# Kernel optimization log

Measured on AMD Instinct MI355X. Metric: run time of the kernel, lower is better.

## Reference

```python
import jax, jax.numpy as jnp
import numpy as np

B, W, D, R = 8, 1024, 1024, 64
GAMMA_MIN, GAMMA_MAX, ALPHA_CAP, EPS = 0.15, 1.0, 1.0, 1e-8


def _linear_init(key, fan_in, shape):
    bound = 1.0 / np.sqrt(fan_in)
    return jax.random.uniform(key, shape, jnp.float32, -bound, bound)


def setup_inputs() -> dict:
    key = jax.random.key(0)
    ks = jax.random.split(key, 12)
    h = jax.random.normal(ks[0], (B, W, D), jnp.float32)
    # k_base init as in __init__: exp(-0.15*max(j-i,0)) * tril, row-normalized
    pos = jnp.arange(W, dtype=jnp.float32)
    dist_ji = jnp.clip(pos[None, :] - pos[:, None], 0.0)
    causal = jnp.tril(jnp.ones((W, W), jnp.float32))
    k_init = jnp.exp(-0.15 * dist_ji) * causal
    k_base = k_init / jnp.clip(k_init.sum(axis=1, keepdims=True), 1e-8)
    # decay_logit init: gammas in [0.95, 0.995] -> inverse sigmoid of normalized gamma
    gammas = jnp.linspace(0.95, 0.995, R)
    graw = jnp.clip((gammas - GAMMA_MIN) / (GAMMA_MAX - GAMMA_MIN), 1e-6, 1 - 1e-6)
    decay_logit = jnp.log(graw / (1.0 - graw))
    return {
        "h": h,
        "k_base": k_base,
        "decay_logit": decay_logit,
        "gate_logit": jnp.asarray(8.0, jnp.float32),
        "alpha_logit": jnp.asarray(0.0, jnp.float32),
        "u": 0.05 * jax.random.normal(ks[1], (D, R), jnp.float32),
        "v": 0.05 * jax.random.normal(ks[2], (D, R), jnp.float32),
        "proj_w": _linear_init(ks[3], D, (D, D)),
        "proj_b": _linear_init(ks[4], D, (D,)),
        "norm1_scale": jnp.ones((D,), jnp.float32),
        "norm2_scale": jnp.ones((D,), jnp.float32),
        "up_w": _linear_init(ks[5], D, (2 * D, D)),
        "up_b": _linear_init(ks[6], D, (2 * D,)),
        "down_w": _linear_init(ks[7], 2 * D, (D, 2 * D)),
        "down_b": _linear_init(ks[8], 2 * D, (D,)),
    }


def _rmsnorm(x, scale):
    return x * jax.lax.rsqrt(jnp.mean(x * x, axis=-1, keepdims=True) + 1e-8) * scale


def _l2norm(x):
    # mirrors F.normalize(x, dim=-1, eps=1e-8)
    n = jnp.sqrt(jnp.sum(x * x, axis=-1, keepdims=True))
    return x / jnp.maximum(n, EPS)


def reference(h, k_base, decay_logit, gate_logit, alpha_logit, u, v,
              proj_w, proj_b, norm1_scale, norm2_scale,
              up_w, up_b, down_w, down_b):
    _, w, _ = h.shape
    pos = jnp.arange(w, dtype=h.dtype)
    causal = jnp.tril(jnp.ones((w, w), h.dtype))          # [W, W]
    dist = jnp.clip(pos[:, None] - pos[None, :], 0.0)     # i - j, clamped >= 0

    residual = h
    h_norm = _rmsnorm(h, norm1_scale)

    # dense k_base path (k_base_rank == 0)
    gate = jax.nn.sigmoid(gate_logit)
    kb = k_base[:w, :w] * causal
    out = gate * jnp.einsum('ij,bjd->bid', kb, h_norm)

    # low-rank q/k with per-rank gamma decay (decay_impl='mask')
    qk = h_norm @ jnp.concatenate((u, v), axis=1)          # [B, W, 2R]
    q_raw, k_raw = jnp.split(qk, [u.shape[1]], axis=-1)
    q = _l2norm(q_raw)
    k = _l2norm(k_raw)

    gamma = GAMMA_MIN + (GAMMA_MAX - GAMMA_MIN) * jax.nn.sigmoid(decay_logit)  # [R]
    log_gamma = jnp.log(jnp.clip(gamma, 1e-8))
    decay_mask = jnp.exp(dist[:, :, None] * log_gamma[None, None, :]) * causal[:, :, None]  # [W, W, R]

    alpha = ALPHA_CAP * jax.nn.sigmoid(alpha_logit)
    # scores[b,i,j] = sum_r q[b,i,r] * decay[i,j,r] * k[b,j,r]
    scores = jnp.einsum('bir,ijr,bjr->bij', q, decay_mask, k)
    out = out + alpha * jnp.einsum('bij,bjd->bid', scores, h_norm)

    h1 = residual + (out @ proj_w.T + proj_b)
    # MLP (GELU exact, mult=2), second residual
    m = _rmsnorm(h1, norm2_scale)
    m = jax.nn.gelu(m @ up_w.T + up_b, approximate=False) @ down_w.T + down_b
    return h1 + m
```

## Files before the change

### kernel.cpp

```cpp
#include <hip/hip_runtime.h>
#include <hip/hip_bf16.h>
#include <math.h>

#define B_ 8
#define W_ 1024
#define D_ 1024
#define R_ 64

typedef __hip_bfloat16 bf16;
typedef __attribute__((ext_vector_type(8))) short bf16x8;
typedef __attribute__((ext_vector_type(4))) float f32x4;

__device__ __forceinline__ float tof(bf16 x) { return __bfloat162float(x); }
__device__ __forceinline__ short f2bs(float f) {
    bf16 b = __float2bfloat16(f);
    return *(short*)&b;
}

__device__ __forceinline__ void async16(const void* g, void* l) {
    __builtin_amdgcn_global_load_lds(
        (const __attribute__((address_space(1))) unsigned int*)g,
        (__attribute__((address_space(3))) unsigned int*)l,
        16, 0, 0);
}

__global__ __launch_bounds__(256)
void rmsnorm_kernel(const float* __restrict__ src, const float* __restrict__ scale,
                    bf16* __restrict__ dst) {
    int row = blockIdx.x;
    const float* x = src + (size_t)row * D_;
    bf16* y = dst + (size_t)row * D_;
    float xv[4];
    float ss = 0.f;
#pragma unroll
    for (int it = 0; it < 4; ++it) {
        int d = threadIdx.x + it * 256;
        xv[it] = x[d];
        ss += xv[it] * xv[it];
    }
#pragma unroll
    for (int off = 32; off; off >>= 1) ss += __shfl_down(ss, off, 64);
    __shared__ float red[4];
    __shared__ float invs;
    int lane = threadIdx.x & 63, wid = threadIdx.x >> 6;
    if (lane == 0) red[wid] = ss;
    __syncthreads();
    if (threadIdx.x == 0) {
        float t = red[0] + red[1] + red[2] + red[3];
        invs = rsqrtf(t / (float)D_ + 1e-8f);
    }
    __syncthreads();
    float inv = invs;
#pragma unroll
    for (int it = 0; it < 4; ++it) {
        int d = threadIdx.x + it * 256;
        y[d] = __float2bfloat16(xv[it] * inv * scale[d]);
    }
}

__global__ __launch_bounds__(256)
void transpose_kernel(const bf16* __restrict__ src, bf16* __restrict__ dst) {
    int b = blockIdx.z;
    int j0 = blockIdx.x * 64, d0 = blockIdx.y * 64;
    __shared__ short Ts[64][72];
    const bf16* S = src + (size_t)b * W_ * D_;
    bf16* Dd = dst + (size_t)b * W_ * D_;
    int tid = threadIdx.x;
    int r = tid >> 3, c = (tid & 7) * 8;
#pragma unroll
    for (int p = 0; p < 2; ++p) {
        int j = r + p * 32;
        bf16x8 vv = *(const bf16x8*)&S[(size_t)(j0 + j) * D_ + d0 + c];
#pragma unroll
        for (int e = 0; e < 8; ++e) Ts[j][c + e] = vv[e];
    }
    __syncthreads();
#pragma unroll
    for (int p = 0; p < 2; ++p) {
        int d = r + p * 32;
        bf16x8 vv;
#pragma unroll
        for (int e = 0; e < 8; ++e) vv[e] = Ts[c + e][d];
        *(bf16x8*)&Dd[(size_t)(d0 + d) * W_ + j0 + c] = vv;
    }
}

__global__ __launch_bounds__(256)
void uvT_kernel(const float* __restrict__ u, const float* __restrict__ v,
                bf16* __restrict__ uvT) {
    int g = blockIdx.z;
    int d0 = blockIdx.x * 64;
    const float* src = g ? v : u;
    __shared__ float Ts[64][65];
    int tid = threadIdx.x;
#pragma unroll
    for (int e = 0; e < 16; ++e) {
        int idx = tid + e * 256;
        int drow = idx >> 6, rcol = idx & 63;
        Ts[drow][rcol] = src[(size_t)(d0 + drow) * 64 + rcol];
    }
    __syncthreads();
#pragma unroll
    for (int e = 0; e < 16; ++e) {
        int idx = tid + e * 256;
        int orow = idx >> 6, ocol = idx & 63;
        uvT[(size_t)(g * 64 + orow) * D_ + d0 + ocol] = __float2bfloat16(Ts[ocol][orow]);
    }
}

__global__ __launch_bounds__(256)
void convert3_kernel(const float* __restrict__ proj, const float* __restrict__ up,
                     const float* __restrict__ down,
                     bf16* __restrict__ projb, bf16* __restrict__ upb,
                     bf16* __restrict__ downb) {
    size_t idx = ((size_t)blockIdx.x * 256 + threadIdx.x) * 8;
    const size_t DD = (size_t)D_ * D_;
    const float* src; bf16* dst; size_t off;
    if (idx < DD)          { src = proj; dst = projb; off = idx; }
    else if (idx < 3 * DD) { src = up;   dst = upb;   off = idx - DD; }
    else                   { src = down; dst = downb; off = idx - 3 * DD; }
    float4 f0 = *(const float4*)(src + off);
    float4 f1 = *(const float4*)(src + off + 4);
    bf16x8 p;
    p[0] = f2bs(f0.x); p[1] = f2bs(f0.y); p[2] = f2bs(f0.z); p[3] = f2bs(f0.w);
    p[4] = f2bs(f1.x); p[5] = f2bs(f1.y); p[6] = f2bs(f1.z); p[7] = f2bs(f1.w);
    *(bf16x8*)(dst + off) = p;
}

__global__ __launch_bounds__(128)
void qk_epilogue_kernel(const float* __restrict__ qkraw,
                        const float* __restrict__ decay_logit,
                        float* __restrict__ qg, float* __restrict__ kg) {
    int row = blockIdx.x;
    int i = row & (W_ - 1);
    int t = threadIdx.x;
    int r = t & 63;
    bool isK = t >= 64;
    const size_t PS = (size_t)B_ * W_ * 128;
    size_t off = (size_t)row * 128 + t;
    float val = qkraw[off] + qkraw[PS + off] + qkraw[2 * PS + off] + qkraw[3 * PS + off];
    float sq = val * val;
#pragma unroll
    for (int o = 32; o; o >>= 1) sq += __shfl_xor(sq, o, 64);
    val = val / fmaxf(sqrtf(sq), 1e-8f);

    float dl = decay_logit[r];
    float gamma = 0.15f + 0.85f * (1.f / (1.f + expf(-dl)));
    float lg = logf(gamma);
    float e = isK ? expf(-(float)i * lg) : expf((float)i * lg);
    float o = val * e;
    if (isK) kg[(size_t)row * R_ + r] = o;
    else     qg[(size_t)row * R_ + r] = o;
}

__global__ __launch_bounds__(256)
void buildM_kernel(const float* __restrict__ qg, const float* __restrict__ kg,
                   const float* __restrict__ k_base,
                   const float* __restrict__ gate_logit,
                   const float* __restrict__ alpha_logit,
                   bf16* __restrict__ M) {
    int b = blockIdx.z;
    int ti = blockIdx.y, tj = blockIdx.x;
    int i0 = ti * 32, j0 = tj * 32;
    int tx = threadIdx.x, ty = threadIdx.y;
    bf16* Mb = M + (size_t)b * W_ * W_;
    const bf16 zero = __float2bfloat16(0.f);

    if (tj > ti) {
#pragma unroll
        for (int a = 0; a < 2; ++a)
#pragma unroll
            for (int c = 0; c < 2; ++c)
                Mb[(size_t)(i0 + ty * 2 + a) * W_ + (j0 + tx * 2 + c)] = zero;
        return;
    }

    __shared__ float Qs[32][65];
    __shared__ float Ks[32][65];
    int tid = ty * 16 + tx;
    for (int e = tid; e < 32 * 64; e += 256) {
        int rr = e & 63, row = e >> 6;
        Qs[row][rr] = qg[((size_t)b * W_ + i0 + row) * R_ + rr];
        Ks[row][rr] = kg[((size_t)b * W_ + j0 + row) * R_ + rr];
    }
    __syncthreads();

    float acc[2][2] = {{0.f, 0.f}, {0.f, 0.f}};
#pragma unroll 8
    for (int r = 0; r < 64; ++r) {
        float qa = Qs[ty * 2 + 0][r], qb = Qs[ty * 2 + 1][r];
        float ka = Ks[tx * 2 + 0][r], kb = Ks[tx * 2 + 1][r];
        acc[0][0] += qa * ka; acc[0][1] += qa * kb;
        acc[1][0] += qb * ka; acc[1][1] += qb * kb;
    }

    float gate  = 1.f / (1.f + expf(-(*gate_logit)));
    float alpha = 1.f / (1.f + expf(-(*alpha_logit)));
#pragma unroll
    for (int a = 0; a < 2; ++a) {
#pragma unroll
        for (int c = 0; c < 2; ++c) {
            int i = i0 + ty * 2 + a, j = j0 + tx * 2 + c;
            float vkb = k_base[(size_t)i * W_ + j];
            float out = (j <= i) ? (gate * vkb + alpha * acc[a][c]) : 0.f;
            Mb[(size_t)i * W_ + j] = __float2bfloat16(out);
        }
    }
}

template<int EPI, int SK>
__global__ __launch_bounds__(512)
void mgemm_kernel(const bf16* __restrict__ A, const bf16* __restrict__ Bm,
                  const float* __restrict__ Res, const float* __restrict__ bias,
                  void* __restrict__ Cout,
                  int M, int N, int K,
                  long sA, long sB, long sC, int causal) {
    __shared__ __align__(16) short At[2][128 * 32];
    __shared__ __align__(16) short Bt[2][128 * 32];
    int z = blockIdx.z;
    const bf16* Ab = (SK > 1) ? A : A + (size_t)z * sA;
    const bf16* Bb = (SK > 1) ? Bm : Bm + (size_t)z * sB;
    int kchunk = K / SK;
    int kbeg = (SK > 1) ? z * kchunk : 0;
    int m0 = blockIdx.x * 128, n0 = blockIdx.y * 128;
    int tid = threadIdx.x;
    int lane = tid & 63, wave = tid >> 6;
    int wy = wave >> 1, wx = wave & 1;
    int quad = lane >> 4, l15 = lane & 15;

    f32x4 acc[2][4];
#pragma unroll
    for (int i = 0; i < 2; ++i)
#pragma unroll
        for (int j = 0; j < 4; ++j)
            acc[i][j] = (f32x4){0.f, 0.f, 0.f, 0.f};

    int kend = kbeg + kchunk;
    if (SK == 1 && causal) kend = (m0 + 128 < K) ? m0 + 128 : K;
    int nIter = (kend - kbeg) >> 5;

    int srcChunk = ((lane & 3) ^ ((lane >> 3) & 3)) * 8;
    size_t rowA = (size_t)(m0 + wave * 16 + (lane >> 2)) * K;
    size_t rowB = (size_t)(n0 + wave * 16 + (lane >> 2)) * K;
    const bf16* aP = Ab + rowA + srcChunk + kbeg;
    const bf16* bP = Bb + rowB + srcChunk + kbeg;
    short* dA[2] = { &At[0][wave * 512], &At[1][wave * 512] };
    short* dB[2] = { &Bt[0][wave * 512], &Bt[1][wave * 512] };

    int rswz = (quad ^ ((l15 >> 1) & 3)) * 8;

    async16(aP, dA[0]);
    async16(bP, dB[0]);
    aP += 32; bP += 32;
    __syncthreads();

    for (int it = 0; it < nIter; ++it) {
        int cur = it & 1;
        if (it + 1 < nIter) {
            int nxt = cur ^ 1;
            async16(aP, dA[nxt]);
            async16(bP, dB[nxt]);
            aP += 32; bP += 32;
        }
        bf16x8 af[2], bfr[4];
#pragma unroll
        for (int mi = 0; mi < 2; ++mi)
            af[mi] = *(const bf16x8*)&At[cur][(wy * 32 + mi * 16 + l15) * 32 + rswz];
#pragma unroll
        for (int ni = 0; ni < 4; ++ni)
            bfr[ni] = *(const bf16x8*)&Bt[cur][(wx * 64 + ni * 16 + l15) * 32 + rswz];
#pragma unroll
        for (int mi = 0; mi < 2; ++mi)
#pragma unroll
            for (int ni = 0; ni < 4; ++ni)
                acc[mi][ni] = __builtin_amdgcn_mfma_f32_16x16x32_bf16(
                    af[mi], bfr[ni], acc[mi][ni], 0, 0, 0);
        __syncthreads();
    }

#pragma unroll
    for (int ni = 0; ni < 4; ++ni) {
        int col = n0 + wx * 64 + ni * 16 + l15;
        float bv = (EPI == 1 || EPI == 2) ? bias[col] : 0.f;
#pragma unroll
        for (int mi = 0; mi < 2; ++mi) {
            int row0 = m0 + wy * 32 + mi * 16 + quad * 4;
#pragma unroll
            for (int r = 0; r < 4; ++r) {
                size_t idx = (size_t)(row0 + r) * N + col;
                float val = acc[mi][ni][r];
                if constexpr (EPI == 0) {
                    ((bf16*)Cout)[(size_t)z * sC + idx] = __float2bfloat16(val);
                } else if constexpr (EPI == 1) {
                    ((float*)Cout)[idx] = val + bv + Res[idx];
                } else if constexpr (EPI == 2) {
                    val += bv;
                    val = 0.5f * val * (1.f + erff(val * 0.70710678118654752f));
                    ((bf16*)Cout)[idx] = __float2bfloat16(val);
                } else {
                    ((float*)Cout)[(size_t)z * sC + idx] = val;
                }
            }
        }
    }
}

extern "C" void kernel_launch(void* const* d_in, const int* in_sizes, int n_in,
                              void* d_out, int out_size, void* d_ws, size_t ws_size,
                              hipStream_t stream) {
    const float* h           = (const float*)d_in[0];
    const float* k_base      = (const float*)d_in[1];
    const float* decay_logit = (const float*)d_in[2];
    const float* gate_logit  = (const float*)d_in[3];
    const float* alpha_logit = (const float*)d_in[4];
    const float* u           = (const float*)d_in[5];
    const float* v           = (const float*)d_in[6];
    const float* proj_w      = (const float*)d_in[7];
    const float* proj_b      = (const float*)d_in[8];
    const float* norm1_scale = (const float*)d_in[9];
    const float* norm2_scale = (const float*)d_in[10];
    const float* up_w        = (const float*)d_in[11];
    const float* up_b        = (const float*)d_in[12];
    const float* down_w      = (const float*)d_in[13];
    const float* down_b      = (const float*)d_in[14];

    const size_t MB = 1048576;
    char* ws = (char*)d_ws;
    bf16*  hnorm   = (bf16*)(ws);
    bf16*  uvT     = (bf16*)(ws + 16 * MB);
    float* qg      = (float*)(ws + 16 * MB);
    float* kg      = (float*)(ws + 18 * MB);
    bf16*  hnormT  = (bf16*)(ws + 20 * MB);
    float* qkraw   = (float*)(ws + 36 * MB);
    bf16*  Mbuf    = (bf16*)(ws + 36 * MB);
    bf16*  proj_wb = (bf16*)(ws + 52 * MB);
    bf16*  up_wb   = (bf16*)(ws + 54 * MB);
    bf16*  down_wb = (bf16*)(ws + 58 * MB);
    bf16*  attn    = hnorm;
    bf16*  mnorm   = hnorm;
    bf16*  tbuf    = hnormT;
    float* h1      = (float*)d_out;

    convert3_kernel<<<5 * D_ * D_ / 2048, 256, 0, stream>>>(
        proj_w, up_w, down_w, proj_wb, up_wb, down_wb);
    uvT_kernel<<<dim3(D_ / 64, 1, 2), 256, 0, stream>>>(u, v, uvT);

    rmsnorm_kernel<<<B_ * W_, 256, 0, stream>>>(h, norm1_scale, hnorm);

    transpose_kernel<<<dim3(W_ / 64, D_ / 64, B_), 256, 0, stream>>>(hnorm, hnormT);

    mgemm_kernel<5, 4><<<dim3(B_ * W_ / 128, 1, 4), 512, 0, stream>>>(
        hnorm, uvT, nullptr, nullptr, qkraw, B_ * W_, 128, D_,
        0, 0, (long)B_ * W_ * 128, 0);

    qk_epilogue_kernel<<<B_ * W_, 128, 0, stream>>>(qkraw, decay_logit, qg, kg);

    buildM_kernel<<<dim3(W_ / 32, W_ / 32, B_), dim3(16, 16), 0, stream>>>(
        qg, kg, k_base, gate_logit, alpha_logit, Mbuf);

    mgemm_kernel<0, 1><<<dim3(W_ / 128, D_ / 128, B_), 512, 0, stream>>>(
        Mbuf, hnormT, nullptr, nullptr, attn, W_, D_, W_,
        (long)W_ * W_, (long)W_ * D_, (long)W_ * D_, 1);

    mgemm_kernel<1, 1><<<dim3(B_ * W_ / 128, D_ / 128, 1), 512, 0, stream>>>(
        attn, proj_wb, h, proj_b, h1, B_ * W_, D_, D_, 0, 0, 0, 0);

    rmsnorm_kernel<<<B_ * W_, 256, 0, stream>>>(h1, norm2_scale, mnorm);

    mgemm_kernel<2, 1><<<dim3(B_ * W_ / 128, 2 * D_ / 128, 1), 512, 0, stream>>>(
        mnorm, up_wb, nullptr, up_b, tbuf, B_ * W_, 2 * D_, D_, 0, 0, 0, 0);

    mgemm_kernel<1, 1><<<dim3(B_ * W_ / 128, D_ / 128, 1), 512, 0, stream>>>(
        tbuf, down_wb, h1, down_b, (float*)d_out, B_ * W_, D_, 2 * D_, 0, 0, 0, 0);
}
```

Measured before the change: 361.6 us.

## Add 256x256-tile pipelined MFMA GEMM kernel for the four large GEMMs

After: 418.8 us. 15.8% more time.

```diff
diff --git a/kernel.cpp b/kernel.cpp
--- a/kernel.cpp
+++ b/kernel.cpp
@@ -305,6 +305,173 @@
     }
 }
 
+#define BAR256() do { __builtin_amdgcn_sched_barrier(0); \
+                      __builtin_amdgcn_s_barrier(); \
+                      __builtin_amdgcn_sched_barrier(0); } while (0)
+#define LGKM0() do { asm volatile("s_waitcnt lgkmcnt(0)" ::: "memory"); \
+                     __builtin_amdgcn_sched_barrier(0); } while (0)
+#define STAGE(IDX, T) do { \
+    const bf16* _g; short* _l; \
+    if ((IDX) < 2) { \
+        _g = aBase + (size_t)((IDX) * 128) * K + (T) * 64; \
+        _l = &At[(T) & 1][(IDX) * 8192 + wave * 1024]; \
+    } else { \
+        _g = bBase + (size_t)(((IDX) - 2) * 128) * K + (T) * 64; \
+        _l = &Bt[(T) & 1][((IDX) - 2) * 8192 + wave * 1024]; \
+    } \
+    async16(_g, _l); \
+    async16(_g + (size_t)8 * K, _l + 512); \
+} while (0)
+#define RD_A(MI, KS) af[MI][KS] = *(const bf16x8*)&Ard[arow + (MI) * 1024 + ck##KS]
+#define RD_B(NI, KS) bfr[NI][KS] = *(const bf16x8*)&Brd[brow + (NI) * 1024 + ck##KS]
+
+template<int EPI>
+__global__ __launch_bounds__(512)
+void mgemm256_kernel(const bf16* __restrict__ A, const bf16* __restrict__ Bm,
+                     const float* __restrict__ Res, const float* __restrict__ bias,
+                     void* __restrict__ Cout,
+                     int M, int N, int K, long sA, long sB, long sC, int causal) {
+    __shared__ __align__(16) short At[2][16384];
+    __shared__ __align__(16) short Bt[2][16384];
+    int z = blockIdx.z;
+    const bf16* Ab = A + (size_t)z * sA;
+    const bf16* Bb = Bm + (size_t)z * sB;
+
+    int bx = blockIdx.x, gx = gridDim.x;
+    if ((gx & 7) == 0) { int cpx = gx >> 3; bx = (bx & 7) * cpx + (bx >> 3); }
+    int m0 = bx * 256, n0 = blockIdx.y * 256;
+
+    int tid = threadIdx.x;
+    int lane = tid & 63, wave = tid >> 6;
+    int wm = wave >> 2, wn = wave & 3;
+    int quad = lane >> 4, l15 = lane & 15;
+
+    f32x4 acc[8][4];
+#pragma unroll
+    for (int i = 0; i < 8; ++i)
+#pragma unroll
+        for (int j = 0; j < 4; ++j)
+            acc[i][j] = (f32x4){0.f, 0.f, 0.f, 0.f};
+
+    int kend = causal ? ((m0 + 256 < K) ? m0 + 256 : K) : K;
+    int NT = kend >> 6;
+
+    const bf16* aBase = Ab + (size_t)(m0 + wave * 16 + (lane >> 3)) * K
+                           + ((lane & 7) ^ (lane >> 3)) * 8;
+    const bf16* bBase = Bb + (size_t)(n0 + wave * 16 + (lane >> 3)) * K
+                           + ((lane & 7) ^ (lane >> 3)) * 8;
+
+    int swz = l15 & 7;
+    int ck0 = (quad ^ swz) * 8;
+    int ck1 = ck0 ^ 32;
+    int arow = (wm * 128 + l15) * 64;
+    int brow = (wn * 64 + l15) * 64;
+
+    STAGE(0, 0); STAGE(1, 0); STAGE(2, 0); STAGE(3, 0);
+    if (NT > 1) {
+        STAGE(0, 1); STAGE(1, 1); STAGE(2, 1);
+        asm volatile("s_waitcnt vmcnt(6)" ::: "memory");
+    } else {
+        asm volatile("s_waitcnt vmcnt(0)" ::: "memory");
+    }
+    BAR256();
+
+    for (int t = 0; t < NT; ++t) {
+        const short* Ard = &At[t & 1][0];
+        const short* Brd = &Bt[t & 1][0];
+        bool i1 = (t + 1 < NT), i2 = (t + 2 < NT);
+        bf16x8 af[8][2], bfr[4][2];
+
+        if (i1) STAGE(3, t + 1);
+        RD_A(0, 0); RD_A(0, 1); RD_A(1, 0); RD_A(1, 1);
+        RD_A(2, 0); RD_A(2, 1); RD_A(3, 0); RD_A(3, 1);
+        RD_A(4, 0); RD_A(4, 1); RD_A(5, 0); RD_A(5, 1);
+        RD_A(6, 0); RD_A(6, 1); RD_A(7, 0); RD_A(7, 1);
+        RD_B(0, 0); RD_B(0, 1); RD_B(1, 0); RD_B(1, 1);
+        BAR256(); LGKM0();
+        __builtin_amdgcn_s_setprio(1);
+#pragma unroll
+        for (int mi = 0; mi < 4; ++mi)
+#pragma unroll
+            for (int ni = 0; ni < 2; ++ni)
+#pragma unroll
+                for (int ks = 0; ks < 2; ++ks)
+                    acc[mi][ni] = __builtin_amdgcn_mfma_f32_16x16x32_bf16(
+                        af[mi][ks], bfr[ni][ks], acc[mi][ni], 0, 0, 0);
+        __builtin_amdgcn_s_setprio(0);
+        BAR256();
+
+        if (i2) STAGE(0, t + 2);
+        RD_B(2, 0); RD_B(2, 1); RD_B(3, 0); RD_B(3, 1);
+        BAR256(); LGKM0();
+        __builtin_amdgcn_s_setprio(1);
+#pragma unroll
+        for (int mi = 0; mi < 4; ++mi)
+#pragma unroll
+            for (int ni = 0; ni < 2; ++ni)
+#pragma unroll
+                for (int ks = 0; ks < 2; ++ks)
+                    acc[mi][2 + ni] = __builtin_amdgcn_mfma_f32_16x16x32_bf16(
+                        af[mi][ks], bfr[2 + ni][ks], acc[mi][2 + ni], 0, 0, 0);
+        __builtin_amdgcn_s_setprio(0);
+        BAR256();
+
+        if (i2) STAGE(1, t + 2);
+        BAR256();
+        __builtin_amdgcn_s_setprio(1);
+#pragma unroll
+        for (int mi = 0; mi < 4; ++mi)
+#pragma unroll
+            for (int ni = 0; ni < 2; ++ni)
+#pragma unroll
+                for (int ks = 0; ks < 2; ++ks)
+                    acc[4 + mi][2 + ni] = __builtin_amdgcn_mfma_f32_16x16x32_bf16(
+                        af[4 + mi][ks], bfr[2 + ni][ks], acc[4 + mi][2 + ni], 0, 0, 0);
+        __builtin_amdgcn_s_setprio(0);
+        BAR256();
+
+        if (i2) STAGE(2, t + 2);
+        if (i2) asm volatile("s_waitcnt vmcnt(6)" ::: "memory");
+        else    asm volatile("s_waitcnt vmcnt(0)" ::: "memory");
+        BAR256();
+        __builtin_amdgcn_s_setprio(1);
+#pragma unroll
+        for (int mi = 0; mi < 4; ++mi)
+#pragma unroll
+            for (int ni = 0; ni < 2; ++ni)
+#pragma unroll
+                for (int ks = 0; ks < 2; ++ks)
+                    acc[4 + mi][ni] = __builtin_amdgcn_mfma_f32_16x16x32_bf16(
+                        af[4 + mi][ks], bfr[ni][ks], acc[4 + mi][ni], 0, 0, 0);
+        __builtin_amdgcn_s_setprio(0);
+        BAR256();
+    }
+
+#pragma unroll
+    for (int ni = 0; ni < 4; ++ni) {
+        int col = n0 + wn * 64 + ni * 16 + l15;
+        float bv = (EPI == 1 || EPI == 2) ? bias[col] : 0.f;
+#pragma unroll
+        for (int mi = 0; mi < 8; ++mi) {
+            int row0 = m0 + wm * 128 + mi * 16 + quad * 4;
+#pragma unroll
+            for (int r = 0; r < 4; ++r) {
+                size_t idx = (size_t)(row0 + r) * N + col;
+                float val = acc[mi][ni][r];
+                if constexpr (EPI == 0) {
+                    ((bf16*)Cout)[(size_t)z * sC + idx] = __float2bfloat16(val);
+                } else if constexpr (EPI == 1) {
+                    ((float*)Cout)[idx] = val + bv + Res[idx];
+                } else {
+                    val += bv;
+                    val = 0.5f * val * (1.f + erff(val * 0.70710678118654752f));
+                    ((bf16*)Cout)[idx] = __float2bfloat16(val);
+                }
+            }
+        }
+    }
+}
+
 extern "C" void kernel_launch(void* const* d_in, const int* in_sizes, int n_in,
                               void* d_out, int out_size, void* d_ws, size_t ws_size,
                               hipStream_t stream) {
@@ -358,18 +525,18 @@
     buildM_kernel<<<dim3(W_ / 32, W_ / 32, B_), dim3(16, 16), 0, stream>>>(
         qg, kg, k_base, gate_logit, alpha_logit, Mbuf);
 
-    mgemm_kernel<0, 1><<<dim3(W_ / 128, D_ / 128, B_), 512, 0, stream>>>(
+    mgemm256_kernel<0><<<dim3(W_ / 256, D_ / 256, B_), 512, 0, stream>>>(
         Mbuf, hnormT, nullptr, nullptr, attn, W_, D_, W_,
         (long)W_ * W_, (long)W_ * D_, (long)W_ * D_, 1);
 
-    mgemm_kernel<1, 1><<<dim3(B_ * W_ / 128, D_ / 128, 1), 512, 0, stream>>>(
+    mgemm256_kernel<1><<<dim3(B_ * W_ / 256, D_ / 256, 1), 512, 0, stream>>>(
         attn, proj_wb, h, proj_b, h1, B_ * W_, D_, D_, 0, 0, 0, 0);
 
     rmsnorm_kernel<<<B_ * W_, 256, 0, stream>>>(h1, norm2_scale, mnorm);
 
-    mgemm_kernel<2, 1><<<dim3(B_ * W_ / 128, 2 * D_ / 128, 1), 512, 0, stream>>>(
+    mgemm256_kernel<2><<<dim3(B_ * W_ / 256, 2 * D_ / 256, 1), 512, 0, stream>>>(
         mnorm, up_wb, nullptr, up_b, tbuf, B_ * W_, 2 * D_, D_, 0, 0, 0, 0);
 
-    mgemm_kernel<1, 1><<<dim3(B_ * W_ / 128, D_ / 128, 1), 512, 0, stream>>>(
+    mgemm256_kernel<1><<<dim3(B_ * W_ / 256, D_ / 256, 1), 512, 0, stream>>>(
         tbuf, down_wb, h1, down_b, (float*)d_out, B_ * W_, D_, 2 * D_, 0, 0, 0, 0);
 }
```

## Deepen GEMM LDS pipeline to four stages with explicit vmcnt waits

Applied to the files above, without the earlier changes.

After: 367.3 us. No clear change (+1.6%).

```diff
diff --git a/kernel.cpp b/kernel.cpp
--- a/kernel.cpp
+++ b/kernel.cpp
@@ -215,8 +215,8 @@
                   void* __restrict__ Cout,
                   int M, int N, int K,
                   long sA, long sB, long sC, int causal) {
-    __shared__ __align__(16) short At[2][128 * 32];
-    __shared__ __align__(16) short Bt[2][128 * 32];
+    __shared__ __align__(16) short At[4][128 * 32];
+    __shared__ __align__(16) short Bt[4][128 * 32];
     int z = blockIdx.z;
     const bf16* Ab = (SK > 1) ? A : A + (size_t)z * sA;
     const bf16* Bb = (SK > 1) ? Bm : Bm + (size_t)z * sB;
@@ -244,38 +244,49 @@
     size_t rowB = (size_t)(n0 + wave * 16 + (lane >> 2)) * K;
     const bf16* aP = Ab + rowA + srcChunk + kbeg;
     const bf16* bP = Bb + rowB + srcChunk + kbeg;
-    short* dA[2] = { &At[0][wave * 512], &At[1][wave * 512] };
-    short* dB[2] = { &Bt[0][wave * 512], &Bt[1][wave * 512] };
+    short* aDst0 = &At[0][0] + wave * 512;
+    short* bDst0 = &Bt[0][0] + wave * 512;
 
     int rswz = (quad ^ ((l15 >> 1) & 3)) * 8;
 
-    async16(aP, dA[0]);
-    async16(bP, dB[0]);
-    aP += 32; bP += 32;
-    __syncthreads();
+    int npro = (nIter < 3) ? nIter : 3;
+    for (int p = 0; p < npro; ++p) {
+        async16(aP, aDst0 + p * 4096);
+        async16(bP, bDst0 + p * 4096);
+        aP += 32; bP += 32;
+    }
 
     for (int it = 0; it < nIter; ++it) {
-        int cur = it & 1;
-        if (it + 1 < nIter) {
-            int nxt = cur ^ 1;
-            async16(aP, dA[nxt]);
-            async16(bP, dB[nxt]);
+        int ahead = nIter - 1 - it;
+        if (ahead >= 2)      asm volatile("s_waitcnt vmcnt(4)" ::: "memory");
+        else if (ahead == 1) asm volatile("s_waitcnt vmcnt(2)" ::: "memory");
+        else                 asm volatile("s_waitcnt vmcnt(0)" ::: "memory");
+        __builtin_amdgcn_sched_barrier(0);
+        __builtin_amdgcn_s_barrier();
+        __builtin_amdgcn_sched_barrier(0);
+
+        if (it + 3 < nIter) {
+            int slot = (it + 3) & 3;
+            async16(aP, aDst0 + slot * 4096);
+            async16(bP, bDst0 + slot * 4096);
             aP += 32; bP += 32;
         }
+
+        const short* Ard = &At[it & 3][0];
+        const short* Brd = &Bt[it & 3][0];
         bf16x8 af[2], bfr[4];
 #pragma unroll
         for (int mi = 0; mi < 2; ++mi)
-            af[mi] = *(const bf16x8*)&At[cur][(wy * 32 + mi * 16 + l15) * 32 + rswz];
+            af[mi] = *(const bf16x8*)&Ard[(wy * 32 + mi * 16 + l15) * 32 + rswz];
 #pragma unroll
         for (int ni = 0; ni < 4; ++ni)
-            bfr[ni] = *(const bf16x8*)&Bt[cur][(wx * 64 + ni * 16 + l15) * 32 + rswz];
+            bfr[ni] = *(const bf16x8*)&Brd[(wx * 64 + ni * 16 + l15) * 32 + rswz];
 #pragma unroll
         for (int mi = 0; mi < 2; ++mi)
 #pragma unroll
             for (int ni = 0; ni < 4; ++ni)
                 acc[mi][ni] = __builtin_amdgcn_mfma_f32_16x16x32_bf16(
                     af[mi], bfr[ni], acc[mi][ni], 0, 0, 0);
-        __syncthreads();
     }
 
 #pragma unroll
```

## Deepen GEMM pipeline to five LDS stages with register double-buffered fragments

Applied to the files above, without the earlier changes.

Result: faster. 350.1 us (-3.2%).

```diff
diff --git a/kernel.cpp b/kernel.cpp
--- a/kernel.cpp
+++ b/kernel.cpp
@@ -208,15 +208,40 @@
     }
 }
 
+#define BAR() do { __builtin_amdgcn_sched_barrier(0); \
+                   __builtin_amdgcn_s_barrier(); \
+                   __builtin_amdgcn_sched_barrier(0); } while (0)
+
+__device__ __forceinline__ void mfma8(const bf16x8 (&fa)[2], const bf16x8 (&fb)[4],
+                                      f32x4 (&acc)[2][4]) {
+#pragma unroll
+    for (int mi = 0; mi < 2; ++mi)
+#pragma unroll
+        for (int ni = 0; ni < 4; ++ni)
+            acc[mi][ni] = __builtin_amdgcn_mfma_f32_16x16x32_bf16(
+                fa[mi], fb[ni], acc[mi][ni], 0, 0, 0);
+}
+
+__device__ __forceinline__ void readf(const short* At0, const short* Bt0, int slot,
+                                      const int (&ao)[2], const int (&bo)[4],
+                                      bf16x8 (&fa)[2], bf16x8 (&fb)[4]) {
+    const short* Ard = At0 + slot * 4096;
+    const short* Brd = Bt0 + slot * 4096;
+#pragma unroll
+    for (int mi = 0; mi < 2; ++mi) fa[mi] = *(const bf16x8*)&Ard[ao[mi]];
+#pragma unroll
+    for (int ni = 0; ni < 4; ++ni) fb[ni] = *(const bf16x8*)&Brd[bo[ni]];
+}
+
 template<int EPI, int SK>
-__global__ __launch_bounds__(512)
+__global__ __launch_bounds__(512, 4)
 void mgemm_kernel(const bf16* __restrict__ A, const bf16* __restrict__ Bm,
                   const float* __restrict__ Res, const float* __restrict__ bias,
                   void* __restrict__ Cout,
                   int M, int N, int K,
                   long sA, long sB, long sC, int causal) {
-    __shared__ __align__(16) short At[2][128 * 32];
-    __shared__ __align__(16) short Bt[2][128 * 32];
+    __shared__ __align__(16) short At[5][128 * 32];
+    __shared__ __align__(16) short Bt[5][128 * 32];
     int z = blockIdx.z;
     const bf16* Ab = (SK > 1) ? A : A + (size_t)z * sA;
     const bf16* Bb = (SK > 1) ? Bm : Bm + (size_t)z * sB;
@@ -244,39 +269,71 @@
     size_t rowB = (size_t)(n0 + wave * 16 + (lane >> 2)) * K;
     const bf16* aP = Ab + rowA + srcChunk + kbeg;
     const bf16* bP = Bb + rowB + srcChunk + kbeg;
-    short* dA[2] = { &At[0][wave * 512], &At[1][wave * 512] };
-    short* dB[2] = { &Bt[0][wave * 512], &Bt[1][wave * 512] };
+    short* aDst = &At[0][0] + wave * 512;
+    short* bDst = &Bt[0][0] + wave * 512;
 
     int rswz = (quad ^ ((l15 >> 1) & 3)) * 8;
-
-    async16(aP, dA[0]);
-    async16(bP, dB[0]);
-    aP += 32; bP += 32;
-    __syncthreads();
-
-    for (int it = 0; it < nIter; ++it) {
-        int cur = it & 1;
-        if (it + 1 < nIter) {
-            int nxt = cur ^ 1;
-            async16(aP, dA[nxt]);
-            async16(bP, dB[nxt]);
-            aP += 32; bP += 32;
-        }
-        bf16x8 af[2], bfr[4];
-#pragma unroll
-        for (int mi = 0; mi < 2; ++mi)
-            af[mi] = *(const bf16x8*)&At[cur][(wy * 32 + mi * 16 + l15) * 32 + rswz];
-#pragma unroll
-        for (int ni = 0; ni < 4; ++ni)
-            bfr[ni] = *(const bf16x8*)&Bt[cur][(wx * 64 + ni * 16 + l15) * 32 + rswz];
-#pragma unroll
-        for (int mi = 0; mi < 2; ++mi)
-#pragma unroll
-            for (int ni = 0; ni < 4; ++ni)
-                acc[mi][ni] = __builtin_amdgcn_mfma_f32_16x16x32_bf16(
-                    af[mi], bfr[ni], acc[mi][ni], 0, 0, 0);
-        __syncthreads();
-    }
+    int ao[2], bo[4];
+#pragma unroll
+    for (int mi = 0; mi < 2; ++mi) ao[mi] = (wy * 32 + mi * 16 + l15) * 32 + rswz;
+#pragma unroll
+    for (int ni = 0; ni < 4; ++ni) bo[ni] = (wx * 64 + ni * 16 + l15) * 32 + rswz;
+
+#pragma unroll
+    for (int p = 0; p < 4; ++p) {
+        async16(aP, aDst + p * 4096);
+        async16(bP, bDst + p * 4096);
+        aP += 32; bP += 32;
+    }
+    asm volatile("s_waitcnt vmcnt(6)" ::: "memory");
+    BAR();
+
+    bf16x8 fa0[2], fb0[4], fa1[2], fb1[4];
+    readf(&At[0][0], &Bt[0][0], 0, ao, bo, fa0, fb0);
+
+    int sStage = 4;
+    int sPf = 1;
+    int nMain = nIter - 4;
+
+    for (int t = 0; t < nMain; t += 2) {
+        asm volatile("s_waitcnt vmcnt(4)" ::: "memory");
+        BAR();
+        async16(aP, aDst + sStage * 4096);
+        async16(bP, bDst + sStage * 4096);
+        aP += 32; bP += 32;
+        sStage = (sStage == 4) ? 0 : sStage + 1;
+        mfma8(fa0, fb0, acc);
+        readf(&At[0][0], &Bt[0][0], sPf, ao, bo, fa1, fb1);
+        sPf = (sPf == 4) ? 0 : sPf + 1;
+        asm volatile("s_waitcnt vmcnt(4)" ::: "memory");
+        BAR();
+        async16(aP, aDst + sStage * 4096);
+        async16(bP, bDst + sStage * 4096);
+        aP += 32; bP += 32;
+        sStage = (sStage == 4) ? 0 : sStage + 1;
+        mfma8(fa1, fb1, acc);
+        readf(&At[0][0], &Bt[0][0], sPf, ao, bo, fa0, fb0);
+        sPf = (sPf == 4) ? 0 : sPf + 1;
+    }
+
+    asm volatile("s_waitcnt vmcnt(4)" ::: "memory");
+    BAR();
+    mfma8(fa0, fb0, acc);
+    readf(&At[0][0], &Bt[0][0], sPf, ao, bo, fa1, fb1);
+    sPf = (sPf == 4) ? 0 : sPf + 1;
+
+    asm volatile("s_waitcnt vmcnt(2)" ::: "memory");
+    BAR();
+    mfma8(fa1, fb1, acc);
+    readf(&At[0][0], &Bt[0][0], sPf, ao, bo, fa0, fb0);
+    sPf = (sPf == 4) ? 0 : sPf + 1;
+
+    asm volatile("s_waitcnt vmcnt(0)" ::: "memory");
+    BAR();
+    mfma8(fa0, fb0, acc);
+    readf(&At[0][0], &Bt[0][0], sPf, ao, bo, fa1, fb1);
+
+    mfma8(fa1, fb1, acc);
 
 #pragma unroll
     for (int ni = 0; ni < 4; ++ni) {
```
